# Kernel optimization log

Measured on AMD Instinct MI355X. Metric: run time of the kernel, lower is better.

## Reference

```python
import jax, jax.numpy as jnp
import numpy as np

B, N, D, H, E = 2, 2048, 256, 8, 65536
SPARSITY = 0.5


def _lin(shape, k):
    return jax.random.normal(k, shape, dtype=jnp.float32) * 0.02


def setup_inputs() -> dict:
    key = jax.random.key(0)
    ks = jax.random.split(key, 16)
    inp = {
        "x": jax.random.normal(ks[0], (B, N, D), dtype=jnp.float32),
        "edge_index": jax.random.randint(ks[1], (2, E), 0, N),
        "q_w": _lin((D, D), ks[2]), "q_b": jnp.zeros((D,), jnp.float32),
        "k_w": _lin((D, D), ks[3]), "k_b": jnp.zeros((D,), jnp.float32),
        "v_w": _lin((D, D), ks[4]), "v_b": jnp.zeros((D,), jnp.float32),
        "o_w": _lin((D, D), ks[5]), "o_b": jnp.zeros((D,), jnp.float32),
        "g1_w": _lin((D // 2, D), ks[6]), "g1_b": jnp.zeros((D // 2,), jnp.float32),
        "g2_w": _lin((1, D // 2), ks[7]), "g2_b": jnp.zeros((1,), jnp.float32),
    }
    return inp


def reference(x, edge_index, q_w, q_b, k_w, k_b, v_w, v_b, o_w, o_b, g1_w, g1_b, g2_w, g2_b):
    b, n, d = x.shape
    hd = d // H
    # topo GNN scores: Linear -> ReLU -> Linear -> [B, N]
    topo = (jax.nn.relu(x @ g1_w.T + g1_b) @ g2_w.T + g2_b)[..., 0]
    Q = (x @ q_w.T + q_b).reshape(b, n, H, hd)
    K = (x @ k_w.T + k_b).reshape(b, n, H, hd)
    V = (x @ v_w.T + v_b).reshape(b, n, H, hd)
    scores = jnp.einsum('bnhd,bmhd->bhnm', Q, K) / np.sqrt(hd).astype(np.float32)
    content_attn = jax.nn.softmax(scores, axis=-1)  # [B, H, N, N]
    # edge mask (shared across batch, as in the torch scatter sparse_mask[:, row, col] = 1)
    edge_mask = jnp.zeros((n, n), jnp.float32).at[edge_index[0], edge_index[1]].set(1.0)
    # topk columns per batch: loop sets same columns for every row -> column mask
    k_top = max(1, int(n * (1.0 - SPARSITY)))
    _, idx = jax.lax.top_k(topo, k_top)  # [B, k_top]
    col_mask = jnp.zeros((b, n), jnp.float32).at[jnp.arange(b)[:, None], idx].set(1.0)
    mask = jnp.maximum(edge_mask[None, :, :], col_mask[:, None, :])  # [B, N, N]
    sparse_attn = content_attn * mask[:, None, :, :]
    sparse_attn = sparse_attn / (sparse_attn.sum(axis=-1, keepdims=True) + 1e-8)
    out = jnp.einsum('bhnm,bmhd->bnhd', sparse_attn, V).reshape(b, n, d)
    out = out @ o_w.T + o_b
    sparse_mask = jnp.broadcast_to(mask[:, None, :, :], (b, H, n, n))
    return out, sparse_mask
```

## Files before the change

kernel.cpp:

```cpp
#include <hip/hip_runtime.h>
#include <hip/hip_bf16.h>

#define BB   2
#define NN   2048
#define DD   256
#define HH   8
#define HD   32
#define EE   65536
#define KTOP 1024
#define NSPLIT 2

typedef __attribute__((ext_vector_type(8))) short bf16x8;
typedef __attribute__((ext_vector_type(4))) float f32x4;

__device__ __forceinline__ float bf2f(unsigned short u) {
    return __uint_as_float(((unsigned)u) << 16);
}
__device__ __forceinline__ unsigned short f2bf(float f) {
    __hip_bfloat16 h = __float2bfloat16(f);
    return *reinterpret_cast<unsigned short*>(&h);
}
__device__ __forceinline__ float loadf(const void* p, int i, int fp) {
    return fp ? ((const float*)p)[i] : bf2f(((const unsigned short*)p)[i]);
}

__device__ __forceinline__ int derive_fp32(const void* x) {
    unsigned wv = ((const unsigned*)x)[threadIdx.x & 63];
    float a = fabsf(bf2f((unsigned short)(wv & 0xFFFFu)));
    float b = fabsf(bf2f((unsigned short)(wv >> 16)));
    bool bad = !(a <= 1e10f && b <= 1e10f);
    return __ballot(bad) != 0ULL;
}

__global__ __launch_bounds__(256) void k_front(
    const void* __restrict__ xraw, const int* __restrict__ ei,
    const void* __restrict__ g1w, const void* __restrict__ g1b,
    const void* __restrict__ g2w, const void* __restrict__ g2b,
    const void* __restrict__ qw, const void* __restrict__ kw,
    const void* __restrict__ vw, const void* __restrict__ ow,
    unsigned short* __restrict__ Xbf,
    unsigned short* __restrict__ qwB, unsigned short* __restrict__ kwB,
    unsigned short* __restrict__ vwB, unsigned short* __restrict__ owB,
    float* __restrict__ topo, unsigned* __restrict__ edgebits)
{
    int blk = blockIdx.x;
    int t = threadIdx.x;
    int fp = derive_fp32(xraw);

    if (blk < 64) {
        const int NV = (BB * NN * DD) / 4;
        for (int i = blk * 256 + t; i < NV; i += 64 * 256) {
            ushort4 o;
            if (fp) {
                float4 v = ((const float4*)xraw)[i];
                o.x = f2bf(v.x); o.y = f2bf(v.y); o.z = f2bf(v.z); o.w = f2bf(v.w);
            } else o = ((const ushort4*)xraw)[i];
            ((ushort4*)Xbf)[i] = o;
        }
    } else if (blk < 80) {
        int p = blk - 64;
        int tsr = p >> 2, sub = p & 3;
        const void* src = (tsr == 0) ? qw : (tsr == 1) ? kw : (tsr == 2) ? vw : ow;
        unsigned short* dst = (tsr == 0) ? qwB : (tsr == 1) ? kwB : (tsr == 2) ? vwB : owB;
        const int NV = (DD * DD) / 4;
        for (int i = sub * 256 + t; i < NV; i += 4 * 256) {
            ushort4 o;
            if (fp) {
                float4 v = ((const float4*)src)[i];
                o.x = f2bf(v.x); o.y = f2bf(v.y); o.z = f2bf(v.z); o.w = f2bf(v.w);
            } else o = ((const ushort4*)src)[i];
            ((ushort4*)dst)[i] = o;
        }
    } else if (blk < 336) {
        __shared__ float xs[16][DD];
        __shared__ float wt[16][129];
        __shared__ float red[16][132];
        int c  = t & 127;
        int rg = t >> 7;
        int row0 = (blk - 80) * 16;

        if (fp) {
            const float4* X4 = (const float4*)xraw + (size_t)row0 * 64;
            for (int i = t; i < 16 * 64; i += 256) {
                int r = i >> 6, k4 = i & 63;
                *reinterpret_cast<float4*>(&xs[r][k4 * 4]) = X4[(size_t)r * 64 + k4];
            }
        } else {
            const ushort4* X4 = (const ushort4*)xraw + (size_t)row0 * 64;
            for (int i = t; i < 16 * 64; i += 256) {
                int r = i >> 6, k4 = i & 63;
                ushort4 u = X4[(size_t)r * 64 + k4];
                xs[r][k4 * 4 + 0] = bf2f(u.x);
                xs[r][k4 * 4 + 1] = bf2f(u.y);
                xs[r][k4 * 4 + 2] = bf2f(u.z);
                xs[r][k4 * 4 + 3] = bf2f(u.w);
            }
        }
        float acc[8];
#pragma unroll
        for (int r = 0; r < 8; ++r) acc[r] = 0.f;

        for (int kt = 0; kt < DD; kt += 16) {
            __syncthreads();
            for (int i = t; i < 128 * 16; i += 256) {
                int nn = i >> 4, kk = i & 15;
                wt[kk][nn] = loadf(g1w, nn * DD + kt + kk, fp);
            }
            __syncthreads();
            float wv[16];
#pragma unroll
            for (int kk = 0; kk < 16; ++kk) wv[kk] = wt[kk][c];
#pragma unroll
            for (int r = 0; r < 8; ++r) {
                const float* xr = &xs[rg * 8 + r][kt];
                float4 x0 = *reinterpret_cast<const float4*>(xr);
                float4 x1 = *reinterpret_cast<const float4*>(xr + 4);
                float4 x2 = *reinterpret_cast<const float4*>(xr + 8);
                float4 x3 = *reinterpret_cast<const float4*>(xr + 12);
                acc[r] += x0.x*wv[0] + x0.y*wv[1] + x0.z*wv[2] + x0.w*wv[3]
                        + x1.x*wv[4] + x1.y*wv[5] + x1.z*wv[6] + x1.w*wv[7]
                        + x2.x*wv[8] + x2.y*wv[9] + x2.z*wv[10] + x2.w*wv[11]
                        + x3.x*wv[12] + x3.y*wv[13] + x3.z*wv[14] + x3.w*wv[15];
            }
        }
        float gb = loadf(g1b, c, fp), gw = loadf(g2w, c, fp);
#pragma unroll
        for (int r = 0; r < 8; ++r)
            red[rg * 8 + r][c] = fmaxf(acc[r] + gb, 0.f) * gw;
        __syncthreads();
        int rr = t >> 4, ii = t & 15;
        float p = 0.f;
#pragma unroll
        for (int j = 0; j < 8; ++j) p += red[rr][ii * 8 + j];
#pragma unroll
        for (int o = 1; o < 16; o <<= 1) p += __shfl_xor(p, o, 64);
        if (ii == 0) topo[row0 + rr] = p + loadf(g2b, 0, fp);
    } else {
        int e = (blk - 336) * 256 + t;
        if (e < EE) {
            int r = ei[e];
            int c = ei[EE + e];
            atomicOr(&edgebits[r * 64 + (c >> 5)], 1u << (c & 31));
        }
    }
}

__global__ __launch_bounds__(256) void k_mid(
    const void* __restrict__ xraw,
    const float* __restrict__ topo, unsigned* __restrict__ colbits,
    const unsigned short* __restrict__ Xb,
    const unsigned short* __restrict__ Wq, const unsigned short* __restrict__ Wk,
    const unsigned short* __restrict__ Wv,
    const void* __restrict__ bq, const void* __restrict__ bk, const void* __restrict__ bv,
    unsigned short* __restrict__ Qo, unsigned short* __restrict__ Ko,
    unsigned short* __restrict__ Vo, float qscale)
{
    int blk = blockIdx.x;
    int t = threadIdx.x;

    if (blk < 16) {
        __shared__ float tl[NN];
        int b = blk >> 3;
        int m = (blk & 7) * 256 + t;
        for (int i = t; i < NN / 4; i += 256)
            *reinterpret_cast<float4*>(&tl[i * 4]) =
                reinterpret_cast<const float4*>(topo + b * NN)[i];
        __syncthreads();
        float v = tl[m];
        int rank = 0;
        for (int j4 = 0; j4 < NN / 4; ++j4) {
            float4 q = *reinterpret_cast<const float4*>(&tl[j4 * 4]);
            int j = j4 * 4;
            rank += (q.x > v) || (q.x == v && (j + 0) < m);
            rank += (q.y > v) || (q.y == v && (j + 1) < m);
            rank += (q.z > v) || (q.z == v && (j + 2) < m);
            rank += (q.w > v) || (q.w == v && (j + 3) < m);
        }
        if (rank < KTOP) atomicOr(&colbits[b * 64 + (m >> 5)], 1u << (m & 31));
        return;
    }

    int fp = derive_fp32(xraw);
    int p = blk - 16;
    int bx = p & 63, by = p >> 6;
    int w = t >> 6, lane = t & 63, q4 = lane >> 4, l16 = lane & 15;
    int m0 = bx * 64 + w * 16;
    int nb = by * 64;

    f32x4 aq[4] = {}, ak[4] = {}, av[4] = {};
#pragma unroll
    for (int ks = 0; ks < 8; ++ks) {
        bf16x8 a = *reinterpret_cast<const bf16x8*>(Xb + (size_t)(m0 + l16) * DD + ks * 32 + q4 * 8);
#pragma unroll
        for (int n = 0; n < 4; ++n) {
            size_t wo = (size_t)(nb + n * 16 + l16) * DD + ks * 32 + q4 * 8;
            bf16x8 b0 = *reinterpret_cast<const bf16x8*>(Wq + wo);
            bf16x8 b1 = *reinterpret_cast<const bf16x8*>(Wk + wo);
            bf16x8 b2 = *reinterpret_cast<const bf16x8*>(Wv + wo);
            aq[n] = __builtin_amdgcn_mfma_f32_16x16x32_bf16(a, b0, aq[n], 0, 0, 0);
            ak[n] = __builtin_amdgcn_mfma_f32_16x16x32_bf16(a, b1, ak[n], 0, 0, 0);
            av[n] = __builtin_amdgcn_mfma_f32_16x16x32_bf16(a, b2, av[n], 0, 0, 0);
        }
    }
#pragma unroll
    for (int n = 0; n < 4; ++n) {
        int col = nb + n * 16 + l16;
        int h = col >> 5, j = col & (HD - 1);
        float bvq = loadf(bq, col, fp), bvk = loadf(bk, col, fp), bvv = loadf(bv, col, fp);
#pragma unroll
        for (int i = 0; i < 4; ++i) {
            int row = m0 + q4 * 4 + i;
            int b = row >> 11, n2 = row & (NN - 1);
            size_t ho = (((size_t)(b * HH + h)) * NN + n2) * HD + j;
            Qo[ho] = f2bf((aq[n][i] + bvq) * qscale);
            Ko[ho] = f2bf(ak[n][i] + bvk);
            Vo[(((size_t)(b * HH + h)) * HD + j) * NN + n2] = f2bf(av[n][i] + bvv);
        }
    }
}

__global__ __launch_bounds__(256) void k_attnmask(
    const void* __restrict__ xraw,
    const unsigned short* __restrict__ Qbf, const unsigned short* __restrict__ Kbf,
    const unsigned short* __restrict__ Vt,
    const unsigned* __restrict__ edgebits, const unsigned* __restrict__ colbits,
    float* __restrict__ Opart, float* __restrict__ Zpart, float* __restrict__ Spart,
    void* __restrict__ dout)
{
    __shared__ unsigned mw[64][33];
    __shared__ short Pl[4][2][16 * 40];
    int blk = blockIdx.x;
    int t = threadIdx.x;

    if (blk >= 1024) {
        int row = blk - 1024;
        int b = row >> 11, n = row & (NN - 1);
        int fp = derive_fp32(xraw);
        unsigned wv = edgebits[n * 64 + (t >> 2)] | colbits[b * 64 + (t >> 2)];
        unsigned bits = (wv >> ((t & 3) * 8)) & 0xFFu;
        if (fp) {
            float v[8];
#pragma unroll
            for (int i = 0; i < 8; ++i) v[i] = ((bits >> i) & 1) ? 1.f : 0.f;
            float* base = (float*)dout + (size_t)BB * NN * DD;
#pragma unroll
            for (int h = 0; h < HH; ++h) {
                size_t idx = ((((size_t)(b * HH + h)) * NN + n) * NN) + (size_t)t * 8;
                *reinterpret_cast<float4*>(base + idx)     = make_float4(v[0], v[1], v[2], v[3]);
                *reinterpret_cast<float4*>(base + idx + 4) = make_float4(v[4], v[5], v[6], v[7]);
            }
        } else {
            unsigned v[8];
#pragma unroll
            for (int i = 0; i < 8; ++i) v[i] = ((bits >> i) & 1) ? 0x3F80u : 0u;
            uint4 o4;
            o4.x = v[0] | (v[1] << 16);
            o4.y = v[2] | (v[3] << 16);
            o4.z = v[4] | (v[5] << 16);
            o4.w = v[6] | (v[7] << 16);
            unsigned short* base = (unsigned short*)dout + (size_t)BB * NN * DD;
#pragma unroll
            for (int h = 0; h < HH; ++h) {
                size_t idx = ((((size_t)(b * HH + h)) * NN + n) * NN) + (size_t)t * 8;
                *reinterpret_cast<uint4*>(base + idx) = o4;
            }
        }
        return;
    }

    int a = blk;
    int split = a & 1;
    int rt    = (a >> 1) & 31;
    int h     = (a >> 6) & 7;
    int b     = a >> 9;
    int w    = t >> 6;
    int lane = t & 63;
    int q4   = lane >> 4;
    int l16  = lane & 15;

    const int r0 = rt * 64;
    const int c0 = split * 32;
    for (int i = t; i < 64 * 32; i += 256) {
        int r = i >> 5, wd = i & 31;
        mw[r][wd] = edgebits[(r0 + r) * 64 + c0 + wd] | colbits[b * 64 + c0 + wd];
    }
    __syncthreads();

    const unsigned short* Qp = Qbf + ((size_t)(b * HH + h)) * NN * HD;
    const unsigned short* Kp = Kbf + ((size_t)(b * HH + h)) * NN * HD;
    const unsigned short* Vp = Vt  + ((size_t)(b * HH + h)) * HD * NN;

    bf16x8 afrag = *reinterpret_cast<const bf16x8*>(Qp + (size_t)(r0 + w * 16 + l16) * HD + q4 * 8);

    f32x4 O0 = {0.f, 0.f, 0.f, 0.f}, O1 = {0.f, 0.f, 0.f, 0.f};
    float Zp[4] = {0.f, 0.f, 0.f, 0.f}, Sp[4] = {0.f, 0.f, 0.f, 0.f};

    bf16x8 kb0, kb1, vb0, vb1;
    {
        int n0 = c0 * 32;
        kb0 = *reinterpret_cast<const bf16x8*>(Kp + (size_t)(n0 + 2 * l16) * HD + q4 * 8);
        kb1 = *reinterpret_cast<const bf16x8*>(Kp + (size_t)(n0 + 2 * l16 + 1) * HD + q4 * 8);
        vb0 = *reinterpret_cast<const bf16x8*>(Vp + (size_t)l16 * NN + n0 + q4 * 8);
        vb1 = *reinterpret_cast<const bf16x8*>(Vp + (size_t)(16 + l16) * NN + n0 + q4 * 8);
    }

    for (int chl = 0; chl < 32; ++chl) {
        int nxt = (chl + 1 < 32) ? chl + 1 : 31;
        int nn0 = (c0 + nxt) * 32;
        bf16x8 nk0 = *reinterpret_cast<const bf16x8*>(Kp + (size_t)(nn0 + 2 * l16) * HD + q4 * 8);
        bf16x8 nk1 = *reinterpret_cast<const bf16x8*>(Kp + (size_t)(nn0 + 2 * l16 + 1) * HD + q4 * 8);
        bf16x8 nv0 = *reinterpret_cast<const bf16x8*>(Vp + (size_t)l16 * NN + nn0 + q4 * 8);
        bf16x8 nv1 = *reinterpret_cast<const bf16x8*>(Vp + (size_t)(16 + l16) * NN + nn0 + q4 * 8);

        f32x4 s0 = __builtin_amdgcn_mfma_f32_16x16x32_bf16(afrag, kb0, (f32x4){0.f,0.f,0.f,0.f}, 0, 0, 0);
        f32x4 s1 = __builtin_amdgcn_mfma_f32_16x16x32_bf16(afrag, kb1, (f32x4){0.f,0.f,0.f,0.f}, 0, 0, 0);

        unsigned* P32 = reinterpret_cast<unsigned*>(&Pl[w][chl & 1][0]);
#pragma unroll
        for (int i = 0; i < 4; ++i) {
            int rl = w * 16 + q4 * 4 + i;
            unsigned wdv = mw[rl][chl];
            float e0 = __expf(s0[i]);
            float e1 = __expf(s1[i]);
            float m0 = ((wdv >> (2 * l16)) & 1u) ? e0 : 0.f;
            float m1 = ((wdv >> (2 * l16 + 1)) & 1u) ? e1 : 0.f;
            Zp[i] += e0 + e1;
            Sp[i] += m0 + m1;
            P32[(q4 * 4 + i) * 20 + l16] =
                (__float_as_uint(m0) >> 16) | (__float_as_uint(m1) & 0xFFFF0000u);
        }
        bf16x8 pfrag = *reinterpret_cast<const bf16x8*>(&Pl[w][chl & 1][l16 * 40 + q4 * 8]);
        O0 = __builtin_amdgcn_mfma_f32_16x16x32_bf16(pfrag, vb0, O0, 0, 0, 0);
        O1 = __builtin_amdgcn_mfma_f32_16x16x32_bf16(pfrag, vb1, O1, 0, 0, 0);

        kb0 = nk0; kb1 = nk1; vb0 = nv0; vb1 = nv1;
    }

#pragma unroll
    for (int o = 1; o < 16; o <<= 1) {
#pragma unroll
        for (int i = 0; i < 4; ++i) {
            Zp[i] += __shfl_xor(Zp[i], o, 64);
            Sp[i] += __shfl_xor(Sp[i], o, 64);
        }
    }
#pragma unroll
    for (int i = 0; i < 4; ++i) {
        int n = r0 + w * 16 + q4 * 4 + i;
        float* op = Opart + (size_t)split * BB * NN * DD + ((size_t)(b * NN + n)) * DD + h * HD;
        op[l16]      = O0[i];
        op[16 + l16] = O1[i];
        if (l16 == 0) {
            size_t zi = (((size_t)(split * BB + b)) * HH + h) * NN + n;
            Zpart[zi] = Zp[i];
            Spart[zi] = Sp[i];
        }
    }
}

__global__ __launch_bounds__(256) void k_projO(
    const void* __restrict__ xraw,
    const float* __restrict__ Opart, const float* __restrict__ Zpart,
    const float* __restrict__ Spart,
    const unsigned short* __restrict__ Wb, const void* __restrict__ bias,
    void* __restrict__ dout)
{
    int t = threadIdx.x;
    int fp = derive_fp32(xraw);
    int w = t >> 6, lane = t & 63, q4 = lane >> 4, l16 = lane & 15;
    int m0 = blockIdx.x * 64 + w * 16;
    int nb = blockIdx.y * 64;
    int arow = m0 + l16;
    int ab = arow >> 11, an = arow & (NN - 1);

    f32x4 acc[4] = {};
#pragma unroll
    for (int ks = 0; ks < 8; ++ks) {
        size_t zi0 = (((size_t)(0 * BB + ab)) * HH + ks) * NN + an;
        size_t zi1 = (((size_t)(1 * BB + ab)) * HH + ks) * NN + an;
        float Zt = Zpart[zi0] + Zpart[zi1];
        float St = Spart[zi0] + Spart[zi1];
        float inv = 1.f / (St + 1e-8f * Zt);
        const float* o0 = Opart + (size_t)arow * DD + ks * 32 + q4 * 8;
        const float* o1 = o0 + (size_t)BB * NN * DD;
        bf16x8 a;
#pragma unroll
        for (int j = 0; j < 8; ++j)
            a[j] = (short)f2bf((o0[j] + o1[j]) * inv);
#pragma unroll
        for (int n = 0; n < 4; ++n) {
            bf16x8 bf = *reinterpret_cast<const bf16x8*>(Wb + (size_t)(nb + n * 16 + l16) * DD + ks * 32 + q4 * 8);
            acc[n] = __builtin_amdgcn_mfma_f32_16x16x32_bf16(a, bf, acc[n], 0, 0, 0);
        }
    }
#pragma unroll
    for (int n = 0; n < 4; ++n) {
        int col = nb + n * 16 + l16;
        float bv = loadf(bias, col, fp);
#pragma unroll
        for (int i = 0; i < 4; ++i) {
            int row = m0 + q4 * 4 + i;
            float v = acc[n][i] + bv;
            if (fp) ((float*)dout)[(size_t)row * DD + col] = v;
            else ((unsigned short*)dout)[(size_t)row * DD + col] = f2bf(v);
        }
    }
}

extern "C" void kernel_launch(void* const* d_in, const int* in_sizes, int n_in,
                              void* d_out, int out_size, void* d_ws, size_t ws_size,
                              hipStream_t stream)
{
    const void* x   = d_in[0];
    const int*  ei  = (const int*)d_in[1];

    char* ws = (char*)d_ws;
    constexpr size_t OFF_EB   = 0;
    constexpr size_t OFF_CB   = OFF_EB  + (size_t)NN * 64 * 4;
    constexpr size_t OFF_TOPO = OFF_CB  + (size_t)BB * 64 * 4;
    constexpr size_t OFF_Q    = OFF_TOPO + (size_t)BB * NN * 4;
    constexpr size_t OFF_K    = OFF_Q   + (size_t)BB * NN * DD * 2;
    constexpr size_t OFF_VT   = OFF_K   + (size_t)BB * NN * DD * 2;
    constexpr size_t OFF_XB   = OFF_VT  + (size_t)BB * NN * DD * 2;
    constexpr size_t OFF_QWB  = OFF_XB  + (size_t)BB * NN * DD * 2;
    constexpr size_t OFF_KWB  = OFF_QWB + (size_t)DD * DD * 2;
    constexpr size_t OFF_VWB  = OFF_KWB + (size_t)DD * DD * 2;
    constexpr size_t OFF_OWB  = OFF_VWB + (size_t)DD * DD * 2;
    constexpr size_t OFF_OP   = OFF_OWB + (size_t)DD * DD * 2;
    constexpr size_t OFF_ZP   = OFF_OP  + (size_t)NSPLIT * BB * NN * DD * 4;
    constexpr size_t OFF_SP   = OFF_ZP  + (size_t)NSPLIT * BB * HH * NN * 4;

    unsigned* edgebits = (unsigned*)(ws + OFF_EB);
    unsigned* colbits  = (unsigned*)(ws + OFF_CB);
    float*    topo     = (float*)(ws + OFF_TOPO);
    unsigned short* Qbf = (unsigned short*)(ws + OFF_Q);
    unsigned short* Kbf = (unsigned short*)(ws + OFF_K);
    unsigned short* Vtb = (unsigned short*)(ws + OFF_VT);
    unsigned short* Xbf = (unsigned short*)(ws + OFF_XB);
    unsigned short* qwB = (unsigned short*)(ws + OFF_QWB);
    unsigned short* kwB = (unsigned short*)(ws + OFF_KWB);
    unsigned short* vwB = (unsigned short*)(ws + OFF_VWB);
    unsigned short* owB = (unsigned short*)(ws + OFF_OWB);
    float*    Opart    = (float*)(ws + OFF_OP);
    float*    Zpart    = (float*)(ws + OFF_ZP);
    float*    Spart    = (float*)(ws + OFF_SP);

    hipMemsetAsync(d_ws, 0, OFF_TOPO, stream);

    k_front<<<dim3(592), dim3(256), 0, stream>>>(
        x, ei, d_in[10], d_in[11], d_in[12], d_in[13],
        d_in[2], d_in[4], d_in[6], d_in[8],
        Xbf, qwB, kwB, vwB, owB, topo, edgebits);

    const float qscale = 0.17677669529663687f;
    k_mid<<<dim3(272), dim3(256), 0, stream>>>(
        x, topo, colbits, Xbf, qwB, kwB, vwB,
        d_in[3], d_in[5], d_in[7], Qbf, Kbf, Vtb, qscale);

    k_attnmask<<<dim3(1024 + BB * NN), dim3(256), 0, stream>>>(
        x, Qbf, Kbf, Vtb, edgebits, colbits, Opart, Zpart, Spart, d_out);

    k_projO<<<dim3(BB * NN / 64, DD / 64), dim3(256), 0, stream>>>(
        x, Opart, Zpart, Spart, owB, d_in[9], d_out);
}
```

Before: 481.5 us.

## Remove key-dimension split in attention and normalize output in-kernel

```diff
diff --git a/kernel.cpp b/kernel.cpp
--- a/kernel.cpp
+++ b/kernel.cpp
@@ -8,7 +8,6 @@
 #define HD   32
 #define EE   65536
 #define KTOP 1024
-#define NSPLIT 2
 
 typedef __attribute__((ext_vector_type(8))) short bf16x8;
 typedef __attribute__((ext_vector_type(4))) float f32x4;
@@ -224,16 +223,15 @@
     const unsigned short* __restrict__ Qbf, const unsigned short* __restrict__ Kbf,
     const unsigned short* __restrict__ Vt,
     const unsigned* __restrict__ edgebits, const unsigned* __restrict__ colbits,
-    float* __restrict__ Opart, float* __restrict__ Zpart, float* __restrict__ Spart,
-    void* __restrict__ dout)
+    unsigned short* __restrict__ AOb, void* __restrict__ dout)
 {
-    __shared__ unsigned mw[64][33];
+    __shared__ unsigned mw[64][65];
     __shared__ short Pl[4][2][16 * 40];
     int blk = blockIdx.x;
     int t = threadIdx.x;
 
-    if (blk >= 1024) {
-        int row = blk - 1024;
+    if (blk >= 512) {
+        int row = blk - 512;
         int b = row >> 11, n = row & (NN - 1);
         int fp = derive_fp32(xraw);
         unsigned wv = edgebits[n * 64 + (t >> 2)] | colbits[b * 64 + (t >> 2)];
@@ -268,21 +266,18 @@
         return;
     }
 
-    int a = blk;
-    int split = a & 1;
-    int rt    = (a >> 1) & 31;
-    int h     = (a >> 6) & 7;
-    int b     = a >> 9;
+    int rt = blk & 31;
+    int h  = (blk >> 5) & 7;
+    int b  = blk >> 8;
     int w    = t >> 6;
     int lane = t & 63;
     int q4   = lane >> 4;
     int l16  = lane & 15;
 
     const int r0 = rt * 64;
-    const int c0 = split * 32;
-    for (int i = t; i < 64 * 32; i += 256) {
-        int r = i >> 5, wd = i & 31;
-        mw[r][wd] = edgebits[(r0 + r) * 64 + c0 + wd] | colbits[b * 64 + c0 + wd];
+    for (int i = t; i < 64 * 64; i += 256) {
+        int r = i >> 6, wd = i & 63;
+        mw[r][wd] = edgebits[(r0 + r) * 64 + wd] | colbits[b * 64 + wd];
     }
     __syncthreads();
 
@@ -297,16 +292,15 @@
 
     bf16x8 kb0, kb1, vb0, vb1;
     {
-        int n0 = c0 * 32;
-        kb0 = *reinterpret_cast<const bf16x8*>(Kp + (size_t)(n0 + 2 * l16) * HD + q4 * 8);
-        kb1 = *reinterpret_cast<const bf16x8*>(Kp + (size_t)(n0 + 2 * l16 + 1) * HD + q4 * 8);
-        vb0 = *reinterpret_cast<const bf16x8*>(Vp + (size_t)l16 * NN + n0 + q4 * 8);
-        vb1 = *reinterpret_cast<const bf16x8*>(Vp + (size_t)(16 + l16) * NN + n0 + q4 * 8);
-    }
-
-    for (int chl = 0; chl < 32; ++chl) {
-        int nxt = (chl + 1 < 32) ? chl + 1 : 31;
-        int nn0 = (c0 + nxt) * 32;
+        kb0 = *reinterpret_cast<const bf16x8*>(Kp + (size_t)(2 * l16) * HD + q4 * 8);
+        kb1 = *reinterpret_cast<const bf16x8*>(Kp + (size_t)(2 * l16 + 1) * HD + q4 * 8);
+        vb0 = *reinterpret_cast<const bf16x8*>(Vp + (size_t)l16 * NN + q4 * 8);
+        vb1 = *reinterpret_cast<const bf16x8*>(Vp + (size_t)(16 + l16) * NN + q4 * 8);
+    }
+
+    for (int chl = 0; chl < 64; ++chl) {
+        int nxt = (chl + 1 < 64) ? chl + 1 : 63;
+        int nn0 = nxt * 32;
         bf16x8 nk0 = *reinterpret_cast<const bf16x8*>(Kp + (size_t)(nn0 + 2 * l16) * HD + q4 * 8);
         bf16x8 nk1 = *reinterpret_cast<const bf16x8*>(Kp + (size_t)(nn0 + 2 * l16 + 1) * HD + q4 * 8);
         bf16x8 nv0 = *reinterpret_cast<const bf16x8*>(Vp + (size_t)l16 * NN + nn0 + q4 * 8);
@@ -346,22 +340,17 @@
     }
 #pragma unroll
     for (int i = 0; i < 4; ++i) {
+        float inv = 1.f / (Sp[i] + 1e-8f * Zp[i]);
         int n = r0 + w * 16 + q4 * 4 + i;
-        float* op = Opart + (size_t)split * BB * NN * DD + ((size_t)(b * NN + n)) * DD + h * HD;
-        op[l16]      = O0[i];
-        op[16 + l16] = O1[i];
-        if (l16 == 0) {
-            size_t zi = (((size_t)(split * BB + b)) * HH + h) * NN + n;
-            Zpart[zi] = Zp[i];
-            Spart[zi] = Sp[i];
-        }
+        unsigned short* op = AOb + ((size_t)(b * NN + n)) * DD + h * HD;
+        op[l16]      = f2bf(O0[i] * inv);
+        op[16 + l16] = f2bf(O1[i] * inv);
     }
 }
 
 __global__ __launch_bounds__(256) void k_projO(
     const void* __restrict__ xraw,
-    const float* __restrict__ Opart, const float* __restrict__ Zpart,
-    const float* __restrict__ Spart,
+    const unsigned short* __restrict__ AOb,
     const unsigned short* __restrict__ Wb, const void* __restrict__ bias,
     void* __restrict__ dout)
 {
@@ -370,23 +359,11 @@
     int w = t >> 6, lane = t & 63, q4 = lane >> 4, l16 = lane & 15;
     int m0 = blockIdx.x * 64 + w * 16;
     int nb = blockIdx.y * 64;
-    int arow = m0 + l16;
-    int ab = arow >> 11, an = arow & (NN - 1);
 
     f32x4 acc[4] = {};
 #pragma unroll
     for (int ks = 0; ks < 8; ++ks) {
-        size_t zi0 = (((size_t)(0 * BB + ab)) * HH + ks) * NN + an;
-        size_t zi1 = (((size_t)(1 * BB + ab)) * HH + ks) * NN + an;
-        float Zt = Zpart[zi0] + Zpart[zi1];
-        float St = Spart[zi0] + Spart[zi1];
-        float inv = 1.f / (St + 1e-8f * Zt);
-        const float* o0 = Opart + (size_t)arow * DD + ks * 32 + q4 * 8;
-        const float* o1 = o0 + (size_t)BB * NN * DD;
-        bf16x8 a;
-#pragma unroll
-        for (int j = 0; j < 8; ++j)
-            a[j] = (short)f2bf((o0[j] + o1[j]) * inv);
+        bf16x8 a = *reinterpret_cast<const bf16x8*>(AOb + (size_t)(m0 + l16) * DD + ks * 32 + q4 * 8);
 #pragma unroll
         for (int n = 0; n < 4; ++n) {
             bf16x8 bf = *reinterpret_cast<const bf16x8*>(Wb + (size_t)(nb + n * 16 + l16) * DD + ks * 32 + q4 * 8);
@@ -422,13 +399,11 @@
     constexpr size_t OFF_K    = OFF_Q   + (size_t)BB * NN * DD * 2;
     constexpr size_t OFF_VT   = OFF_K   + (size_t)BB * NN * DD * 2;
     constexpr size_t OFF_XB   = OFF_VT  + (size_t)BB * NN * DD * 2;
-    constexpr size_t OFF_QWB  = OFF_XB  + (size_t)BB * NN * DD * 2;
+    constexpr size_t OFF_AOB  = OFF_XB  + (size_t)BB * NN * DD * 2;
+    constexpr size_t OFF_QWB  = OFF_AOB + (size_t)BB * NN * DD * 2;
     constexpr size_t OFF_KWB  = OFF_QWB + (size_t)DD * DD * 2;
     constexpr size_t OFF_VWB  = OFF_KWB + (size_t)DD * DD * 2;
     constexpr size_t OFF_OWB  = OFF_VWB + (size_t)DD * DD * 2;
-    constexpr size_t OFF_OP   = OFF_OWB + (size_t)DD * DD * 2;
-    constexpr size_t OFF_ZP   = OFF_OP  + (size_t)NSPLIT * BB * NN * DD * 4;
-    constexpr size_t OFF_SP   = OFF_ZP  + (size_t)NSPLIT * BB * HH * NN * 4;
 
     unsigned* edgebits = (unsigned*)(ws + OFF_EB);
     unsigned* colbits  = (unsigned*)(ws + OFF_CB);
@@ -437,13 +412,11 @@
     unsigned short* Kbf = (unsigned short*)(ws + OFF_K);
     unsigned short* Vtb = (unsigned short*)(ws + OFF_VT);
     unsigned short* Xbf = (unsigned short*)(ws + OFF_XB);
+    unsigned short* AOb = (unsigned short*)(ws + OFF_AOB);
     unsigned short* qwB = (unsigned short*)(ws + OFF_QWB);
     unsigned short* kwB = (unsigned short*)(ws + OFF_KWB);
     unsigned short* vwB = (unsigned short*)(ws + OFF_VWB);
     unsigned short* owB = (unsigned short*)(ws + OFF_OWB);
-    float*    Opart    = (float*)(ws + OFF_OP);
-    float*    Zpart    = (float*)(ws + OFF_ZP);
-    float*    Spart    = (float*)(ws + OFF_SP);
 
     hipMemsetAsync(d_ws, 0, OFF_TOPO, stream);
 
@@ -457,9 +430,9 @@
         x, topo, colbits, Xbf, qwB, kwB, vwB,
         d_in[3], d_in[5], d_in[7], Qbf, Kbf, Vtb, qscale);
 
-    k_attnmask<<<dim3(1024 + BB * NN), dim3(256), 0, stream>>>(
-        x, Qbf, Kbf, Vtb, edgebits, colbits, Opart, Zpart, Spart, d_out);
+    k_attnmask<<<dim3(512 + BB * NN), dim3(256), 0, stream>>>(
+        x, Qbf, Kbf, Vtb, edgebits, colbits, AOb, d_out);
 
     k_projO<<<dim3(BB * NN / 64, DD / 64), dim3(256), 0, stream>>>(
-        x, Opart, Zpart, Spart, owB, d_in[9], d_out);
-}
+        x, AOb, owB, d_in[9], d_out);
+}
```

After: 447.6 us. 1.08x faster.
